# Performance work log

Measured on AMD Instinct MI355X. Metric: run time of the kernel, lower is better.

Reference implementation:

```python
import jax, jax.numpy as jnp
import numpy as np

L, N, C, OPL = 20, 512, 10, 13        # levels, nodes/level, conditions/node, condition op length
HID, MID = 512, 256                   # hidden_dim, hid_dim
OP_DIM, EX_DIM, SAMP_DIM = 15, 108, 1000
EPS = 1e-5


def _lstm_cell(x, h, c, wih, whh, bih, bhh):
    gates = x @ wih.T + h @ whh.T + bih + bhh
    i, f, g, o = jnp.split(gates, 4, axis=-1)  # torch gate order i,f,g,o
    c = jax.nn.sigmoid(f) * c + jax.nn.sigmoid(i) * jnp.tanh(g)
    h = jax.nn.sigmoid(o) * jnp.tanh(c)
    return h, c


def _batchnorm(x, g, b):  # training-mode BatchNorm1d (biased batch stats)
    m = x.mean(0)
    v = x.var(0)
    return (x - m) / jnp.sqrt(v + EPS) * g + b


def setup_inputs() -> dict:
    key = jax.random.key(0)
    ks = iter(jax.random.split(key, 48))
    rn = lambda shp, s=1.0: jax.random.normal(next(ks), shp, jnp.float32) * s
    ru = lambda shp: jax.random.uniform(next(ks), shp, jnp.float32)
    w = lambda shp: rn(shp, 0.05)
    inp = {
        'operators': ru((L, N, OP_DIM)),
        'extra_infos': rn((L, N, EX_DIM)),
        'condition1s': rn((L, N, C, OPL)),
        'condition2s': rn((L, N, C, OPL)),
        'samples': ru((L, N, SAMP_DIM)),
        'condition_masks': jnp.ones((L, N, 1), jnp.float32),
        'mapping': jax.random.randint(next(ks), (L, 2, N), 0, N + 1),
        # lstm1 (condition encoder)
        'w_ih1': w((4 * HID, OPL)), 'w_hh1': w((4 * HID, HID)),
        'b_ih1': w((4 * HID,)), 'b_hh1': w((4 * HID,)),
        # mlps feeding the tree lstm
        'sample_w': w((MID, SAMP_DIM)), 'sample_b': w((MID,)),
        'cond_w': w((MID, HID)), 'cond_b': w((MID,)),
        'bn1_g': jnp.ones((MID,), jnp.float32), 'bn1_b': jnp.zeros((MID,), jnp.float32),
        # lstm2 (tree aggregation)
        'w_ih2': w((4 * HID, OP_DIM + EX_DIM + 2 * MID)), 'w_hh2': w((4 * HID, HID)),
        'b_ih2': w((4 * HID,)), 'b_hh2': w((4 * HID,)),
        'bn2_g': jnp.ones((HID,), jnp.float32), 'bn2_b': jnp.zeros((HID,), jnp.float32),
        # task heads
        't1_w2': w((MID, HID)), 't1_b2': w((MID,)),
        't2_w2': w((MID, HID)), 't2_b2': w((MID,)),
        'bn3_g': jnp.ones((MID,), jnp.float32), 'bn3_b': jnp.zeros((MID,), jnp.float32),
        't1_w3': w((MID, MID)), 't1_b3': w((MID,)),
        't2_w3': w((MID, MID)), 't2_b3': w((MID,)),
        't1_ow': w((1, MID)), 't1_ob': w((1,)),
        't2_ow': w((1, MID)), 't2_ob': w((1,)),
    }
    return inp


def reference(operators, extra_infos, condition1s, condition2s, samples, condition_masks, mapping,
              w_ih1, w_hh1, b_ih1, b_hh1, sample_w, sample_b, cond_w, cond_b, bn1_g, bn1_b,
              w_ih2, w_hh2, b_ih2, b_hh2, bn2_g, bn2_b,
              t1_w2, t1_b2, t2_w2, t2_b2, bn3_g, bn3_b,
              t1_w3, t1_b3, t2_w3, t2_b3, t1_ow, t1_ob, t2_ow, t2_ob):
    Lv, Np = operators.shape[0], operators.shape[1]
    mapping = mapping.astype(jnp.int32)

    # --- condition encoder: lstm1 over each node's predicate sequence ---
    x = condition1s.reshape(Lv * Np, C, OPL)
    h0 = jnp.zeros((Lv * Np, HID), operators.dtype)

    def step1(carry, xt):
        h, c = carry
        h, c = _lstm_cell(xt, h, c, w_ih1, w_hh1, b_ih1, b_hh1)
        return (h, c), None

    (h_last, _), _ = jax.lax.scan(step1, (h0, h0), jnp.swapaxes(x, 0, 1))
    cond = _batchnorm(jax.nn.relu(h_last @ cond_w.T + cond_b), bn1_g, bn1_b)
    cond = cond.reshape(Lv, Np, MID)

    samp = jax.nn.relu(samples @ sample_w.T + sample_b) * condition_masks
    feats = jnp.concatenate([operators, extra_infos, cond, samp], axis=2)  # [L, N, 123+2*MID]

    # --- bottom level: lstm2 single step from zero state ---
    z0 = jnp.zeros((Np, HID), feats.dtype)
    hid, cid = _lstm_cell(feats[Lv - 1], z0, z0, w_ih2, w_hh2, b_ih2, b_hh2)

    # --- bottom-up tree aggregation: gather children states, average, lstm2 step ---
    def level_step(carry, inputs):
        hid, cid = carry
        x_lvl, mapp = inputs  # x_lvl [N, F], mapp [2, N], index 0 == pad (no child)
        pad = jnp.zeros((1, HID), hid.dtype)
        nh = jnp.concatenate([pad, hid], axis=0)  # [N+1, H]
        nc = jnp.concatenate([pad, cid], axis=0)
        h = (nh[mapp[0]] + nh[mapp[1]]) * 0.5
        c = (nc[mapp[0]] + nc[mapp[1]]) * 0.5
        hid, cid = _lstm_cell(x_lvl, h, c, w_ih2, w_hh2, b_ih2, b_hh2)
        return (hid, cid), None

    xs = (feats[Lv - 2::-1], mapping[Lv - 2::-1])
    (hid, cid), _ = jax.lax.scan(level_step, (hid, cid), xs)

    # --- heads (batch_size == Np: all level-0 nodes active for these inputs) ---
    z = _batchnorm(hid, bn2_g, bn2_b)
    t1 = _batchnorm(jax.nn.relu(z @ t1_w2.T + t1_b2), bn3_g, bn3_b)
    t1 = jax.nn.sigmoid(jax.nn.relu(t1 @ t1_w3.T + t1_b3) @ t1_ow.T + t1_ob)
    t2 = _batchnorm(jax.nn.relu(z @ t2_w2.T + t2_b2), bn3_g, bn3_b)
    t2 = jax.nn.sigmoid(jax.nn.relu(t2 @ t2_w3.T + t2_b3) @ t2_ow.T + t2_ob)
    return t1, t2
```

## Files before the change

kernel.cpp:

```cpp
#include <hip/hip_runtime.h>
#include <hip/hip_bf16.h>


typedef __bf16 bf16x8 __attribute__((ext_vector_type(8)));
typedef float f32x4 __attribute__((ext_vector_type(4)));

#define MROWS 10240
#define LDH1  552
#define L1_ROWS 48
#define L1_BLOCKS 214

#define PF_BIAS1   0
#define PF_BIAS2   2048
#define PF_CONDB   4096
#define PF_SAMPB   4352
#define PF_BCAT2   4608
#define PF_B3CAT   5120
#define PF_BN1G    5632
#define PF_BN1B    5888
#define PF_BN2G    6144
#define PF_BN2B    6656
#define PF_BN3G    7168
#define PF_BN3B    7424
#define PF_OW      7680
#define PF_OB      8192
#define PF_TOTAL   8194

__device__ __forceinline__ float fsig(float x) {
  return __builtin_amdgcn_rcpf(1.0f + __expf(-x));
}
__device__ __forceinline__ float ftanh(float x) {
  return fmaf(2.0f, __builtin_amdgcn_rcpf(1.0f + __expf(-2.0f * x)), -1.0f);
}
__device__ __forceinline__ bf16x8 bzero8() {
  bf16x8 z;
#pragma unroll
  for (int i = 0; i < 8; ++i) z[i] = (__bf16)0.0f;
  return z;
}
__device__ __forceinline__ float ld_in(const void* p, long i, int bf) {
  return bf ? (float)((const __bf16*)p)[i] : ((const float*)p)[i];
}

__global__ void detect_kernel(const unsigned* __restrict__ masks, int* __restrict__ flag) {
  if (blockIdx.x == 0 && threadIdx.x == 0)
    *flag = (masks[0] == 0x3F803F80u) ? 1 : 0;
}

__global__ void prep_kernel(const int* __restrict__ flagp,
    const void* w_ih1, const void* w_hh1, const void* b_ih1, const void* b_hh1,
    const void* w_ih2, const void* w_hh2, const void* b_ih2, const void* b_hh2,
    const void* t1_w2, const void* t2_w2, const void* t1_b2, const void* t2_b2,
    const void* cond_w, const void* cond_b, const void* sample_w, const void* sample_b,
    const void* bn1_g, const void* bn1_b, const void* bn2_g, const void* bn2_b,
    const void* bn3_g, const void* bn3_b,
    const void* t1_w3, const void* t1_b3, const void* t2_w3, const void* t2_b3,
    const void* t1_ow, const void* t1_ob, const void* t2_ow, const void* t2_ob,
    const void* masks,
    __bf16* __restrict__ w1s, __bf16* __restrict__ w2s,
    __bf16* __restrict__ wcat2, __bf16* __restrict__ cond_w_bf,
    __bf16* __restrict__ sample_w_bf, __bf16* __restrict__ w3cat_bf,
    float* __restrict__ mask_f, float* __restrict__ pf)
{
  const int bf = *flagp;
  const int S1 = 2048 * 544;
  const int S2 = 2048 * 1152;
  const int S3 = 512 * 512;
  const int S4 = 256 * 512;
  const int S5 = 256 * 1000;
  const int S6 = 512 * 256;
  const int S7 = 10240;
  const int total = S1 + S2 + S3 + S4 + S5 + S6 + S7 + PF_TOTAL;
  for (int idx = blockIdx.x * blockDim.x + threadIdx.x; idx < total;
       idx += gridDim.x * blockDim.x) {
    int i = idx;
    if (i < S1) {
      int e = i & 7, l = (i >> 3) & 63, g = (i >> 9) & 3;
      int grp = i >> 11;
      int kk = grp % 17, cgt = grp / 17;
      int colq = l & 15, quad = l >> 4;
      int row = g * 512 + cgt * 16 + colq;
      int k = kk * 32 + quad * 8 + e;
      float v = (k < 512) ? ld_in(w_hh1, (long)row * 512 + k, bf)
              : (k < 525) ? ld_in(w_ih1, (long)row * 13 + (k - 512), bf) : 0.0f;
      w1s[i] = (__bf16)v;
      continue;
    }
    i -= S1;
    if (i < S2) {
      int e = i & 7, l = (i >> 3) & 63, g = (i >> 9) & 3;
      int grp = i >> 11;
      int kk = grp % 36, jt = grp / 36;
      int colq = l & 15, quad = l >> 4;
      int row = g * 512 + jt * 16 + colq;
      int k = kk * 32 + quad * 8 + e;
      float v = (k < 635) ? ld_in(w_ih2, (long)row * 635 + k, bf)
              : (k < 640) ? 0.0f : ld_in(w_hh2, (long)row * 512 + (k - 640), bf);
      w2s[i] = (__bf16)v;
      continue;
    }
    i -= S2;
    if (i < S3) {
      int r = i >> 9, k = i & 511;
      wcat2[i] = (__bf16)((r < 256) ? ld_in(t1_w2, r * 512 + k, bf)
                                    : ld_in(t2_w2, (r - 256) * 512 + k, bf));
      continue;
    }
    i -= S3;
    if (i < S4) { cond_w_bf[i] = (__bf16)ld_in(cond_w, i, bf); continue; }
    i -= S4;
    if (i < S5) { sample_w_bf[i] = (__bf16)ld_in(sample_w, i, bf); continue; }
    i -= S5;
    if (i < S6) {
      int r = i >> 8, k = i & 255;
      w3cat_bf[i] = (__bf16)((r < 256) ? ld_in(t1_w3, r * 256 + k, bf)
                                       : ld_in(t2_w3, (r - 256) * 256 + k, bf));
      continue;
    }
    i -= S6;
    if (i < S7) { mask_f[i] = ld_in(masks, i, bf); continue; }
    i -= S7;
    {
      int j = i;
      float v;
      if      (j < 2048) v = ld_in(b_ih1, j, bf) + ld_in(b_hh1, j, bf);
      else if (j < 4096) v = ld_in(b_ih2, j - 2048, bf) + ld_in(b_hh2, j - 2048, bf);
      else if (j < 4352) v = ld_in(cond_b, j - 4096, bf);
      else if (j < 4608) v = ld_in(sample_b, j - 4352, bf);
      else if (j < 5120) { int k = j - 4608; v = (k < 256) ? ld_in(t1_b2, k, bf) : ld_in(t2_b2, k - 256, bf); }
      else if (j < 5632) { int k = j - 5120; v = (k < 256) ? ld_in(t1_b3, k, bf) : ld_in(t2_b3, k - 256, bf); }
      else if (j < 5888) v = ld_in(bn1_g, j - 5632, bf);
      else if (j < 6144) v = ld_in(bn1_b, j - 5888, bf);
      else if (j < 6656) v = ld_in(bn2_g, j - 6144, bf);
      else if (j < 7168) v = ld_in(bn2_b, j - 6656, bf);
      else if (j < 7424) v = ld_in(bn3_g, j - 7168, bf);
      else if (j < 7680) v = ld_in(bn3_b, j - 7424, bf);
      else if (j < 8192) { int k = j - 7680; v = (k < 256) ? ld_in(t1_ow, k, bf) : ld_in(t2_ow, k - 256, bf); }
      else v = (j == 8192) ? ld_in(t1_ob, 0, bf) : ld_in(t2_ob, 0, bf);
      pf[j] = v;
    }
  }
}

__global__ void conv_samples_kernel(const int* __restrict__ flagp,
                                    const void* __restrict__ samples,
                                    __bf16* __restrict__ dst)
{
  const int bf = *flagp;
  if (bf) return;
  for (long i = blockIdx.x * blockDim.x + threadIdx.x; i < 10240000L;
       i += (long)gridDim.x * blockDim.x)
    dst[i] = (__bf16)ld_in(samples, i, bf);
}

__global__ void featcopy_kernel(const int* __restrict__ flagp,
                                const void* __restrict__ ops,
                                const void* __restrict__ extra,
                                __bf16* __restrict__ Astage)
{
  const int bf = *flagp;
  int idx = blockIdx.x * blockDim.x + threadIdx.x;
  int m = idx >> 7, c = idx & 127;
  float v; int col;
  if (c < 15)       { v = ld_in(ops, (long)m * 15 + c, bf);            col = c; }
  else if (c < 123) { v = ld_in(extra, (long)m * 108 + (c - 15), bf);  col = c; }
  else              { v = 0.0f;                                        col = 512 + c; }
  Astage[(size_t)m * 640 + col] = (__bf16)v;
}

__global__ __launch_bounds__(1024, 4) void lstm1_kernel(
    const int* __restrict__ flagp,
    const void* __restrict__ cond1,
    const __bf16* __restrict__ w1s,
    const float*  __restrict__ bias,
    __bf16* __restrict__ h_out)
{
  __shared__ __attribute__((aligned(16))) __bf16 hbuf[2][L1_ROWS * LDH1];
  const int bf   = *flagp;
  const int tid  = threadIdx.x;
  const int wave = tid >> 6;
  const int lane = tid & 63;
  const int colq = lane & 15;
  const int quad = lane >> 4;
  const int r0   = blockIdx.x * L1_ROWS;

  {
    bf16x8 z8 = bzero8();
    for (int i = tid * 8; i < 2 * L1_ROWS * LDH1; i += 1024 * 8)
      *(bf16x8*)&hbuf[0][i] = z8;
  }
  __syncthreads();
  if (tid < L1_ROWS * 8) {
    int row = tid >> 3, jj = tid & 7;
    int gr = r0 + row;
    if (gr < MROWS) {
      long base = (long)gr * 130;
      hbuf[0][row * LDH1 + 512 + jj] = (__bf16)ld_in(cond1, base + jj, bf);
      if (jj < 5) hbuf[0][row * LDH1 + 520 + jj] = (__bf16)ld_in(cond1, base + 8 + jj, bf);
    }
  }
  __syncthreads();

  float c_reg[2][3][4];
#pragma unroll
  for (int a = 0; a < 2; ++a)
#pragma unroll
    for (int b = 0; b < 3; ++b)
#pragma unroll
      for (int r = 0; r < 4; ++r) c_reg[a][b][r] = 0.0f;

  const int jbase = wave * 32;

  float bI[2], bF[2], bG[2], bO[2];
#pragma unroll
  for (int cg = 0; cg < 2; ++cg) {
    const int j = jbase + cg * 16 + colq;
    bI[cg] = bias[j];
    bF[cg] = bias[512 + j];
    bG[cg] = bias[1024 + j];
    bO[cg] = bias[1536 + j];
  }

#pragma unroll 1
  for (int t = 0; t < 10; ++t) {
    const __bf16* hcur = hbuf[t & 1];
    __bf16* hnxt = hbuf[(t + 1) & 1];
#pragma unroll
    for (int cg = 0; cg < 2; ++cg) {
      const int jc = jbase + cg * 16;
      f32x4 acc[3][4];
#pragma unroll
      for (int a = 0; a < 3; ++a)
#pragma unroll
        for (int g = 0; g < 4; ++g)
#pragma unroll
          for (int r = 0; r < 4; ++r) acc[a][g][r] = 0.0f;

      const __bf16* wp = w1s + ((size_t)(wave * 2 + cg) * 17 * 4 * 512) + (lane << 3);
#pragma unroll 1
      for (int kk = 0; kk < 17; ++kk) {
        const int kof = (kk << 5) + (quad << 3);
        bf16x8 af[3];
#pragma unroll
        for (int rt = 0; rt < 3; ++rt)
          af[rt] = *(const bf16x8*)&hcur[(rt * 16 + colq) * LDH1 + kof];
        bf16x8 bfr[4];
#pragma unroll
        for (int g = 0; g < 4; ++g)
          bfr[g] = *(const bf16x8*)&wp[(kk * 4 + g) << 9];
#pragma unroll
        for (int g = 0; g < 4; ++g)
#pragma unroll
          for (int rt = 0; rt < 3; ++rt)
            acc[rt][g] = __builtin_amdgcn_mfma_f32_16x16x32_bf16(af[rt], bfr[g], acc[rt][g], 0, 0, 0);
      }
#pragma unroll
      for (int rt = 0; rt < 3; ++rt)
#pragma unroll
        for (int r = 0; r < 4; ++r) {
          float c = fsig(acc[rt][1][r] + bF[cg]) * c_reg[cg][rt][r]
                  + fsig(acc[rt][0][r] + bI[cg]) * ftanh(acc[rt][2][r] + bG[cg]);
          c_reg[cg][rt][r] = c;
          float h = fsig(acc[rt][3][r] + bO[cg]) * ftanh(c);
          hnxt[(rt * 16 + quad * 4 + r) * LDH1 + jc + colq] = (__bf16)h;
        }
    }
    if (t < 9 && tid < L1_ROWS * 8) {
      int row = tid >> 3, jj = tid & 7;
      int gr = r0 + row;
      if (gr < MROWS) {
        long base = ((long)gr * 10 + (t + 1)) * 13;
        hnxt[row * LDH1 + 512 + jj] = (__bf16)ld_in(cond1, base + jj, bf);
        if (jj < 5) hnxt[row * LDH1 + 520 + jj] = (__bf16)ld_in(cond1, base + 8 + jj, bf);
      }
    }
    __syncthreads();
  }

  for (int i = tid; i < L1_ROWS * 64; i += 1024) {
    int row = i >> 6;
    int cb  = (i & 63) << 3;
    *(bf16x8*)&h_out[(size_t)(r0 + row) * 512 + cb] = *(const bf16x8*)&hbuf[0][row * LDH1 + cb];
  }
}

template<int ACT, int OUTBF, int MASKED>
__global__ __launch_bounds__(256, 4) void gemm_kernel(
    const __bf16* __restrict__ A, int lda,
    const __bf16* __restrict__ W, int ldw,
    const float* __restrict__ bias,
    float* __restrict__ outf, __bf16* __restrict__ outb, int ldc,
    const float* __restrict__ mask, int K)
{
  const int tid  = threadIdx.x;
  const int wave = tid >> 6;
  const int lane = tid & 63;
  const int colq = lane & 15;
  const int quad = lane >> 4;
  const int m0 = blockIdx.y * 64 + (wave >> 1) * 32;
  const int n0 = blockIdx.x * 64 + (wave & 1) * 32;

  f32x4 acc[2][2];
#pragma unroll
  for (int a = 0; a < 2; ++a)
#pragma unroll
    for (int b = 0; b < 2; ++b)
#pragma unroll
      for (int r = 0; r < 4; ++r) acc[a][b][r] = 0.0f;

  const int nk = (K + 31) >> 5;
  for (int kk = 0; kk < nk; ++kk) {
    const int kof = (kk << 5) + (quad << 3);
    bf16x8 a0, a1, b0, b1;
    if (kof < K) {
      a0 = *(const bf16x8*)&A[(size_t)(m0 + colq) * lda + kof];
      a1 = *(const bf16x8*)&A[(size_t)(m0 + 16 + colq) * lda + kof];
      b0 = *(const bf16x8*)&W[(size_t)(n0 + colq) * ldw + kof];
      b1 = *(const bf16x8*)&W[(size_t)(n0 + 16 + colq) * ldw + kof];
    } else {
      a0 = bzero8(); a1 = a0; b0 = a0; b1 = a0;
    }
    acc[0][0] = __builtin_amdgcn_mfma_f32_16x16x32_bf16(a0, b0, acc[0][0], 0, 0, 0);
    acc[0][1] = __builtin_amdgcn_mfma_f32_16x16x32_bf16(a0, b1, acc[0][1], 0, 0, 0);
    acc[1][0] = __builtin_amdgcn_mfma_f32_16x16x32_bf16(a1, b0, acc[1][0], 0, 0, 0);
    acc[1][1] = __builtin_amdgcn_mfma_f32_16x16x32_bf16(a1, b1, acc[1][1], 0, 0, 0);
  }
#pragma unroll
  for (int ai = 0; ai < 2; ++ai)
#pragma unroll
    for (int bi = 0; bi < 2; ++bi) {
      const int col = n0 + bi * 16 + colq;
      const float bv = bias[col];
#pragma unroll
      for (int r = 0; r < 4; ++r) {
        const int row = m0 + ai * 16 + quad * 4 + r;
        float v = acc[ai][bi][r] + bv;
        if (ACT) v = fmaxf(v, 0.0f);
        if (MASKED) v *= mask[row];
        if (OUTBF) outb[(size_t)row * ldc + col] = (__bf16)v;
        else       outf[(size_t)row * ldc + col] = v;
      }
    }
}

__global__ __launch_bounds__(256, 4) void sampgemm_kernel(
    const int* __restrict__ flagp,
    const void* __restrict__ samples_raw,
    const __bf16* __restrict__ samp_bf,
    const __bf16* __restrict__ W,
    const float* __restrict__ bias,
    __bf16* __restrict__ outb,
    const float* __restrict__ mask)
{
  const __bf16* A = (*flagp) ? (const __bf16*)samples_raw : samp_bf;
  const int tid  = threadIdx.x;
  const int wave = tid >> 6;
  const int lane = tid & 63;
  const int colq = lane & 15;
  const int quad = lane >> 4;
  const int m0 = blockIdx.y * 64 + (wave >> 1) * 32;
  const int n0 = blockIdx.x * 64 + (wave & 1) * 32;
  const int K = 1000;

  f32x4 acc[2][2];
#pragma unroll
  for (int a = 0; a < 2; ++a)
#pragma unroll
    for (int b = 0; b < 2; ++b)
#pragma unroll
      for (int r = 0; r < 4; ++r) acc[a][b][r] = 0.0f;

  for (int kk = 0; kk < 32; ++kk) {
    const int kof = (kk << 5) + (quad << 3);
    bf16x8 a0, a1, b0, b1;
    if (kof < K) {
      a0 = *(const bf16x8*)&A[(size_t)(m0 + colq) * 1000 + kof];
      a1 = *(const bf16x8*)&A[(size_t)(m0 + 16 + colq) * 1000 + kof];
      b0 = *(const bf16x8*)&W[(size_t)(n0 + colq) * 1000 + kof];
      b1 = *(const bf16x8*)&W[(size_t)(n0 + 16 + colq) * 1000 + kof];
    } else {
      a0 = bzero8(); a1 = a0; b0 = a0; b1 = a0;
    }
    acc[0][0] = __builtin_amdgcn_mfma_f32_16x16x32_bf16(a0, b0, acc[0][0], 0, 0, 0);
    acc[0][1] = __builtin_amdgcn_mfma_f32_16x16x32_bf16(a0, b1, acc[0][1], 0, 0, 0);
    acc[1][0] = __builtin_amdgcn_mfma_f32_16x16x32_bf16(a1, b0, acc[1][0], 0, 0, 0);
    acc[1][1] = __builtin_amdgcn_mfma_f32_16x16x32_bf16(a1, b1, acc[1][1], 0, 0, 0);
  }
#pragma unroll
  for (int ai = 0; ai < 2; ++ai)
#pragma unroll
    for (int bi = 0; bi < 2; ++bi) {
      const int col = n0 + bi * 16 + colq;
      const float bv = bias[col];
#pragma unroll
      for (int r = 0; r < 4; ++r) {
        const int row = m0 + ai * 16 + quad * 4 + r;
        float v = fmaxf(acc[ai][bi][r] + bv, 0.0f) * mask[row];
        outb[(size_t)row * 640 + col] = (__bf16)v;
      }
    }
}

__global__ __launch_bounds__(256, 4) void treelvl_kernel(
    const __bf16* __restrict__ Alvl,
    const __bf16* __restrict__ w2s,
    const float* __restrict__ bias,
    const int* __restrict__ mapping,
    const __bf16* __restrict__ h_src, const float* __restrict__ c_src,
    __bf16* __restrict__ h_dst, float* __restrict__ c_dst,
    float* __restrict__ h_f32, int first)
{
  const int tid  = threadIdx.x;
  const int wv   = tid >> 6;
  const int lane = tid & 63;
  const int colq = lane & 15;
  const int quad = lane >> 4;
  const int jt = blockIdx.x;
  const int mt = blockIdx.y;
  const int rowA = mt * 64 + wv * 16 + colq;

  int i0 = 0, i1 = 0;
  if (!first) { i0 = mapping[rowA]; i1 = mapping[512 + rowA]; }
  const float s0 = (i0 > 0) ? 0.5f : 0.0f;
  const float s1 = (i1 > 0) ? 0.5f : 0.0f;
  const __bf16* h0p = h_src + (size_t)((i0 > 0 ? i0 : 1) - 1) * 512;
  const __bf16* h1p = h_src + (size_t)((i1 > 0 ? i1 : 1) - 1) * 512;

  f32x4 acc[4];
#pragma unroll
  for (int g = 0; g < 4; ++g)
#pragma unroll
    for (int r = 0; r < 4; ++r) acc[g][r] = 0.0f;

  const __bf16* wbase = w2s + (size_t)jt * 36 * 4 * 512 + (lane << 3);
  const __bf16* arow  = Alvl + (size_t)rowA * 640;

#pragma unroll 4
  for (int kk = 0; kk < 20; ++kk) {
    const int kof = (kk << 5) + (quad << 3);
    bf16x8 afr = *(const bf16x8*)&arow[kof];
    bf16x8 b0 = *(const bf16x8*)&wbase[(kk * 4 + 0) << 9];
    bf16x8 b1 = *(const bf16x8*)&wbase[(kk * 4 + 1) << 9];
    bf16x8 b2 = *(const bf16x8*)&wbase[(kk * 4 + 2) << 9];
    bf16x8 b3 = *(const bf16x8*)&wbase[(kk * 4 + 3) << 9];
    acc[0] = __builtin_amdgcn_mfma_f32_16x16x32_bf16(afr, b0, acc[0], 0, 0, 0);
    acc[1] = __builtin_amdgcn_mfma_f32_16x16x32_bf16(afr, b1, acc[1], 0, 0, 0);
    acc[2] = __builtin_amdgcn_mfma_f32_16x16x32_bf16(afr, b2, acc[2], 0, 0, 0);
    acc[3] = __builtin_amdgcn_mfma_f32_16x16x32_bf16(afr, b3, acc[3], 0, 0, 0);
  }
#pragma unroll 4
  for (int kk = 20; kk < 36; ++kk) {
    const int kh = ((kk - 20) << 5) + (quad << 3);
    bf16x8 v0 = *(const bf16x8*)&h0p[kh];
    bf16x8 v1 = *(const bf16x8*)&h1p[kh];
    bf16x8 afr;
#pragma unroll
    for (int e = 0; e < 8; ++e)
      afr[e] = (__bf16)((float)v0[e] * s0 + (float)v1[e] * s1);
    bf16x8 b0 = *(const bf16x8*)&wbase[(kk * 4 + 0) << 9];
    bf16x8 b1 = *(const bf16x8*)&wbase[(kk * 4 + 1) << 9];
    bf16x8 b2 = *(const bf16x8*)&wbase[(kk * 4 + 2) << 9];
    bf16x8 b3 = *(const bf16x8*)&wbase[(kk * 4 + 3) << 9];
    acc[0] = __builtin_amdgcn_mfma_f32_16x16x32_bf16(afr, b0, acc[0], 0, 0, 0);
    acc[1] = __builtin_amdgcn_mfma_f32_16x16x32_bf16(afr, b1, acc[1], 0, 0, 0);
    acc[2] = __builtin_amdgcn_mfma_f32_16x16x32_bf16(afr, b2, acc[2], 0, 0, 0);
    acc[3] = __builtin_amdgcn_mfma_f32_16x16x32_bf16(afr, b3, acc[3], 0, 0, 0);
  }

  const int j = jt * 16 + colq;
  const float bi  = bias[j];
  const float bff = bias[512 + j];
  const float bg  = bias[1024 + j];
  const float bo  = bias[1536 + j];
#pragma unroll
  for (int r = 0; r < 4; ++r) {
    const int mrow = mt * 64 + wv * 16 + quad * 4 + r;
    float ci = 0.0f;
    if (!first) {
      int a0 = mapping[mrow], a1 = mapping[512 + mrow];
      if (a0 > 0) ci += c_src[(size_t)(a0 - 1) * 512 + j];
      if (a1 > 0) ci += c_src[(size_t)(a1 - 1) * 512 + j];
      ci *= 0.5f;
    }
    float c = fsig(acc[1][r] + bff) * ci + fsig(acc[0][r] + bi) * ftanh(acc[2][r] + bg);
    float h = fsig(acc[3][r] + bo) * ftanh(c);
    h_dst[(size_t)mrow * 512 + j] = (__bf16)h;
    c_dst[(size_t)mrow * 512 + j] = c;
    h_f32[(size_t)mrow * 512 + j] = h;
  }
}

__global__ void stats1_kernel(const float* __restrict__ in, int ld, int N,
                              int rows_per_blk, float* __restrict__ partial)
{
  int b = blockIdx.x;
  int r0 = b * rows_per_blk;
  for (int c = threadIdx.x; c < N; c += blockDim.x) {
    float s = 0.0f, sq = 0.0f;
    for (int r = 0; r < rows_per_blk; ++r) {
      float v = in[(size_t)(r0 + r) * ld + c];
      s += v; sq += v * v;
    }
    partial[(size_t)(2 * b) * N + c] = s;
    partial[(size_t)(2 * b + 1) * N + c] = sq;
  }
}

__global__ void stats2_kernel(const float* __restrict__ partial, int nb, int N,
                              float invM, float* __restrict__ stats)
{
  int c = blockIdx.x * blockDim.x + threadIdx.x;
  if (c >= N) return;
  float s = 0.0f, sq = 0.0f;
  for (int b = 0; b < nb; ++b) {
    s  += partial[(size_t)(2 * b) * N + c];
    sq += partial[(size_t)(2 * b + 1) * N + c];
  }
  float mean = s * invM;
  float var  = sq * invM - mean * mean;
  stats[c]     = mean;
  stats[N + c] = rsqrtf(fmaxf(var, 0.0f) + 1e-5f);
}

__global__ void norm_kernel(const float* __restrict__ in, int ldin,
                            const float* __restrict__ stats, int N, int cshift, int gmask,
                            const float* __restrict__ g, const float* __restrict__ b,
                            __bf16* __restrict__ outp, int ldc, int total)
{
  for (int idx = blockIdx.x * blockDim.x + threadIdx.x; idx < total;
       idx += gridDim.x * blockDim.x) {
    int row = idx >> cshift;
    int c = idx & (N - 1);
    float v = (in[(size_t)row * ldin + c] - stats[c]) * stats[N + c];
    int gi = c & gmask;
    v = v * g[gi] + b[gi];
    outp[(size_t)row * ldc + c] = (__bf16)v;
  }
}

__global__ void head_kernel(const int* __restrict__ flagp,
                            const __bf16* __restrict__ tmp3,
                            const float* __restrict__ pf,
                            void* __restrict__ outp)
{
  const int bf = *flagp;
  int idx = blockIdx.x * blockDim.x + threadIdx.x;
  if (idx >= 1024) return;
  int which = idx >> 9;
  int n = idx & 511;
  const __bf16* row = tmp3 + (size_t)n * 512 + which * 256;
  const float* ow = pf + PF_OW + which * 256;
  float s = pf[PF_OB + which];
  for (int k = 0; k < 256; ++k) s += (float)row[k] * ow[k];
  float v = fsig(s);
  if (bf) ((__bf16*)outp)[idx] = (__bf16)v;
  else    ((float*)outp)[idx]  = v;
}

extern "C" void kernel_launch(void* const* d_in, const int* in_sizes, int n_in,
                              void* d_out, int out_size, void* d_ws, size_t ws_size,
                              hipStream_t stream) {
  const void* operators       = d_in[0];
  const void* extra_infos     = d_in[1];
  const void* condition1s     = d_in[2];
  const void* samples         = d_in[4];
  const void* condition_masks = d_in[5];
  const int*  mapping         = (const int*)d_in[6];
  (void)in_sizes; (void)n_in; (void)out_size; (void)ws_size;

  char* ws = (char*)d_ws;
  size_t off = 0;
  auto alloc = [&](size_t bytes) -> void* {
    void* p = ws + off;
    off += (bytes + 255) & ~(size_t)255;
    return p;
  };
  int*    flag     = (int*)   alloc(256);
  __bf16* w1s      = (__bf16*)alloc((size_t)2048 * 544 * 2);
  __bf16* w2s      = (__bf16*)alloc((size_t)2048 * 1152 * 2);
  __bf16* wcat2    = (__bf16*)alloc(512 * 512 * 2);
  __bf16* cond_w_bf   = (__bf16*)alloc(256 * 512 * 2);
  __bf16* sample_w_bf = (__bf16*)alloc(256 * 1000 * 2);
  __bf16* w3cat_bf    = (__bf16*)alloc(512 * 256 * 2);
  float*  mask_f   = (float*) alloc(10240 * 4);
  float*  pf       = (float*) alloc(PF_TOTAL * 4);
  __bf16* samp_bf  = (__bf16*)alloc((size_t)10240 * 1000 * 2);
  __bf16* h_last   = (__bf16*)alloc((size_t)10272 * 512 * 2);
  float*  condtmp  = (float*) alloc((size_t)10240 * 256 * 4);
  __bf16* Astage   = (__bf16*)alloc((size_t)20 * 512 * 640 * 2);
  __bf16* hs0      = (__bf16*)alloc(512 * 512 * 2);
  __bf16* hs1      = (__bf16*)alloc(512 * 512 * 2);
  float*  cs0      = (float*) alloc(512 * 512 * 4);
  float*  cs1      = (float*) alloc(512 * 512 * 4);
  float*  h_f32    = (float*) alloc(512 * 512 * 4);
  __bf16* zbuf     = (__bf16*)alloc(512 * 512 * 2);
  float*  tmp1     = (float*) alloc(512 * 512 * 4);
  __bf16* tmp2     = (__bf16*)alloc(512 * 512 * 2);
  __bf16* tmp3     = (__bf16*)alloc(512 * 512 * 2);
  float*  partial  = (float*) alloc(64 * 2 * 512 * 4);
  float*  statsb   = (float*) alloc(2 * 512 * 4);

  detect_kernel<<<1, 64, 0, stream>>>((const unsigned*)condition_masks, flag);
  prep_kernel<<<4096, 256, 0, stream>>>(flag,
      d_in[7], d_in[8], d_in[9], d_in[10],
      d_in[17], d_in[18], d_in[19], d_in[20],
      d_in[23], d_in[25], d_in[24], d_in[26],
      d_in[13], d_in[14], d_in[11], d_in[12],
      d_in[15], d_in[16], d_in[21], d_in[22],
      d_in[27], d_in[28],
      d_in[29], d_in[30], d_in[31], d_in[32],
      d_in[33], d_in[34], d_in[35], d_in[36],
      condition_masks,
      w1s, w2s, wcat2, cond_w_bf, sample_w_bf, w3cat_bf, mask_f, pf);
  conv_samples_kernel<<<4096, 256, 0, stream>>>(flag, samples, samp_bf);
  featcopy_kernel<<<5120, 256, 0, stream>>>(flag, operators, extra_infos, Astage);
  lstm1_kernel<<<L1_BLOCKS, 1024, 0, stream>>>(flag, condition1s, w1s, pf + PF_BIAS1, h_last);

  gemm_kernel<1,0,0><<<dim3(4,160), 256, 0, stream>>>(h_last, 512, cond_w_bf, 512,
      pf + PF_CONDB, condtmp, nullptr, 256, nullptr, 512);
  stats1_kernel<<<64, 256, 0, stream>>>(condtmp, 256, 256, 160, partial);
  stats2_kernel<<<1, 256, 0, stream>>>(partial, 64, 256, 1.0f / 10240.0f, statsb);
  norm_kernel<<<2560, 256, 0, stream>>>(condtmp, 256, statsb, 256, 8, 255,
      pf + PF_BN1G, pf + PF_BN1B, Astage + 123, 640, 10240 * 256);

  sampgemm_kernel<<<dim3(4,160), 256, 0, stream>>>(flag, samples, samp_bf,
      sample_w_bf, pf + PF_SAMPB, Astage + 379, mask_f);

  for (int lvl = 19; lvl >= 0; --lvl) {
    __bf16* hd = (lvl & 1) ? hs1 : hs0;
    float*  cd = (lvl & 1) ? cs1 : cs0;
    const __bf16* hsrc = (lvl & 1) ? hs0 : hs1;
    const float*  csrc = (lvl & 1) ? cs0 : cs1;
    treelvl_kernel<<<dim3(32,8), 256, 0, stream>>>(
        Astage + (size_t)lvl * 512 * 640, w2s, pf + PF_BIAS2,
        mapping + lvl * 1024, hsrc, csrc, hd, cd, h_f32, (lvl == 19) ? 1 : 0);
  }

  stats1_kernel<<<8, 256, 0, stream>>>(h_f32, 512, 512, 64, partial);
  stats2_kernel<<<2, 256, 0, stream>>>(partial, 8, 512, 1.0f / 512.0f, statsb);
  norm_kernel<<<256, 256, 0, stream>>>(h_f32, 512, statsb, 512, 9, 511,
      pf + PF_BN2G, pf + PF_BN2B, zbuf, 512, 512 * 512);

  gemm_kernel<1,0,0><<<dim3(8,8), 256, 0, stream>>>(zbuf, 512, wcat2, 512,
      pf + PF_BCAT2, tmp1, nullptr, 512, nullptr, 512);
  stats1_kernel<<<8, 256, 0, stream>>>(tmp1, 512, 512, 64, partial);
  stats2_kernel<<<2, 256, 0, stream>>>(partial, 8, 512, 1.0f / 512.0f, statsb);
  norm_kernel<<<256, 256, 0, stream>>>(tmp1, 512, statsb, 512, 9, 255,
      pf + PF_BN3G, pf + PF_BN3B, tmp2, 512, 512 * 512);

  gemm_kernel<1,1,0><<<dim3(4,8), 256, 0, stream>>>(tmp2, 512, w3cat_bf, 256,
      pf + PF_B3CAT, nullptr, tmp3, 512, nullptr, 256);
  gemm_kernel<1,1,0><<<dim3(4,8), 256, 0, stream>>>(tmp2 + 256, 512, w3cat_bf + 256 * 256, 256,
      pf + PF_B3CAT + 256, nullptr, tmp3 + 256, 512, nullptr, 256);

  head_kernel<<<4, 256, 0, stream>>>(flag, tmp3, pf, d_out);
}
```

Before: 1.027 ms.

## Fuse tree-level LSTM launches into one cooperative kernel with grid sync

Replaces 20 per-level tree LSTM kernel launches with a single cooperative kernel that loops over levels and uses grid.sync between them. Launch overhead and inter-kernel gaps are removed, and the f32 hidden copy is written only at the final level. The cost is a grid-wide barrier per level, and the kernel requires all 256 blocks to be co-resident. It also drops __restrict__ qualifiers, which may affect codegen.

```diff
diff --git a/kernel.cpp b/kernel.cpp
--- a/kernel.cpp
+++ b/kernel.cpp
@@ -1,5 +1,8 @@
 #include <hip/hip_runtime.h>
 #include <hip/hip_bf16.h>
+#include <hip/hip_cooperative_groups.h>
+
+namespace cg = cooperative_groups;
 
 
 typedef __bf16 bf16x8 __attribute__((ext_vector_type(8)));
@@ -401,15 +404,16 @@
     }
 }
 
-__global__ __launch_bounds__(256, 4) void treelvl_kernel(
-    const __bf16* __restrict__ Alvl,
-    const __bf16* __restrict__ w2s,
-    const float* __restrict__ bias,
-    const int* __restrict__ mapping,
-    const __bf16* __restrict__ h_src, const float* __restrict__ c_src,
-    __bf16* __restrict__ h_dst, float* __restrict__ c_dst,
-    float* __restrict__ h_f32, int first)
-{
+__global__ __launch_bounds__(256, 4) void tree_kernel(
+    const __bf16* Astage,
+    const __bf16* w2s,
+    const float*  bias,
+    const int*    mapping_all,
+    __bf16* hs0, __bf16* hs1,
+    float*  cs0, float*  cs1,
+    float*  h_f32)
+{
+  cg::grid_group grid = cg::this_grid();
   const int tid  = threadIdx.x;
   const int wv   = tid >> 6;
   const int lane = tid & 63;
@@ -418,75 +422,90 @@
   const int jt = blockIdx.x;
   const int mt = blockIdx.y;
   const int rowA = mt * 64 + wv * 16 + colq;
-
-  int i0 = 0, i1 = 0;
-  if (!first) { i0 = mapping[rowA]; i1 = mapping[512 + rowA]; }
-  const float s0 = (i0 > 0) ? 0.5f : 0.0f;
-  const float s1 = (i1 > 0) ? 0.5f : 0.0f;
-  const __bf16* h0p = h_src + (size_t)((i0 > 0 ? i0 : 1) - 1) * 512;
-  const __bf16* h1p = h_src + (size_t)((i1 > 0 ? i1 : 1) - 1) * 512;
-
-  f32x4 acc[4];
-#pragma unroll
-  for (int g = 0; g < 4; ++g)
-#pragma unroll
-    for (int r = 0; r < 4; ++r) acc[g][r] = 0.0f;
+  const int mrow0 = mt * 64 + wv * 16 + quad * 4;
 
   const __bf16* wbase = w2s + (size_t)jt * 36 * 4 * 512 + (lane << 3);
-  const __bf16* arow  = Alvl + (size_t)rowA * 640;
-
-#pragma unroll 4
-  for (int kk = 0; kk < 20; ++kk) {
-    const int kof = (kk << 5) + (quad << 3);
-    bf16x8 afr = *(const bf16x8*)&arow[kof];
-    bf16x8 b0 = *(const bf16x8*)&wbase[(kk * 4 + 0) << 9];
-    bf16x8 b1 = *(const bf16x8*)&wbase[(kk * 4 + 1) << 9];
-    bf16x8 b2 = *(const bf16x8*)&wbase[(kk * 4 + 2) << 9];
-    bf16x8 b3 = *(const bf16x8*)&wbase[(kk * 4 + 3) << 9];
-    acc[0] = __builtin_amdgcn_mfma_f32_16x16x32_bf16(afr, b0, acc[0], 0, 0, 0);
-    acc[1] = __builtin_amdgcn_mfma_f32_16x16x32_bf16(afr, b1, acc[1], 0, 0, 0);
-    acc[2] = __builtin_amdgcn_mfma_f32_16x16x32_bf16(afr, b2, acc[2], 0, 0, 0);
-    acc[3] = __builtin_amdgcn_mfma_f32_16x16x32_bf16(afr, b3, acc[3], 0, 0, 0);
-  }
-#pragma unroll 4
-  for (int kk = 20; kk < 36; ++kk) {
-    const int kh = ((kk - 20) << 5) + (quad << 3);
-    bf16x8 v0 = *(const bf16x8*)&h0p[kh];
-    bf16x8 v1 = *(const bf16x8*)&h1p[kh];
-    bf16x8 afr;
-#pragma unroll
-    for (int e = 0; e < 8; ++e)
-      afr[e] = (__bf16)((float)v0[e] * s0 + (float)v1[e] * s1);
-    bf16x8 b0 = *(const bf16x8*)&wbase[(kk * 4 + 0) << 9];
-    bf16x8 b1 = *(const bf16x8*)&wbase[(kk * 4 + 1) << 9];
-    bf16x8 b2 = *(const bf16x8*)&wbase[(kk * 4 + 2) << 9];
-    bf16x8 b3 = *(const bf16x8*)&wbase[(kk * 4 + 3) << 9];
-    acc[0] = __builtin_amdgcn_mfma_f32_16x16x32_bf16(afr, b0, acc[0], 0, 0, 0);
-    acc[1] = __builtin_amdgcn_mfma_f32_16x16x32_bf16(afr, b1, acc[1], 0, 0, 0);
-    acc[2] = __builtin_amdgcn_mfma_f32_16x16x32_bf16(afr, b2, acc[2], 0, 0, 0);
-    acc[3] = __builtin_amdgcn_mfma_f32_16x16x32_bf16(afr, b3, acc[3], 0, 0, 0);
-  }
-
   const int j = jt * 16 + colq;
   const float bi  = bias[j];
   const float bff = bias[512 + j];
   const float bg  = bias[1024 + j];
   const float bo  = bias[1536 + j];
-#pragma unroll
-  for (int r = 0; r < 4; ++r) {
-    const int mrow = mt * 64 + wv * 16 + quad * 4 + r;
-    float ci = 0.0f;
-    if (!first) {
-      int a0 = mapping[mrow], a1 = mapping[512 + mrow];
-      if (a0 > 0) ci += c_src[(size_t)(a0 - 1) * 512 + j];
-      if (a1 > 0) ci += c_src[(size_t)(a1 - 1) * 512 + j];
-      ci *= 0.5f;
-    }
-    float c = fsig(acc[1][r] + bff) * ci + fsig(acc[0][r] + bi) * ftanh(acc[2][r] + bg);
-    float h = fsig(acc[3][r] + bo) * ftanh(c);
-    h_dst[(size_t)mrow * 512 + j] = (__bf16)h;
-    c_dst[(size_t)mrow * 512 + j] = c;
-    h_f32[(size_t)mrow * 512 + j] = h;
+
+#pragma unroll 1
+  for (int lvl = 19; lvl >= 0; --lvl) {
+    const int first = (lvl == 19);
+    const __bf16* Alvl = Astage + (size_t)lvl * 512 * 640;
+    const int* mapping = mapping_all + lvl * 1024;
+    __bf16* h_dst = (lvl & 1) ? hs1 : hs0;
+    float*  c_dst = (lvl & 1) ? cs1 : cs0;
+    const __bf16* h_src = (lvl & 1) ? hs0 : hs1;
+    const float*  c_src = (lvl & 1) ? cs0 : cs1;
+
+    int i0 = 0, i1 = 0;
+    if (!first) { i0 = mapping[rowA]; i1 = mapping[512 + rowA]; }
+    const float s0 = (i0 > 0) ? 0.5f : 0.0f;
+    const float s1 = (i1 > 0) ? 0.5f : 0.0f;
+    const __bf16* h0p = h_src + (size_t)((i0 > 0 ? i0 : 1) - 1) * 512;
+    const __bf16* h1p = h_src + (size_t)((i1 > 0 ? i1 : 1) - 1) * 512;
+
+    f32x4 acc[4];
+#pragma unroll
+    for (int g = 0; g < 4; ++g)
+#pragma unroll
+      for (int r = 0; r < 4; ++r) acc[g][r] = 0.0f;
+
+    const __bf16* arow = Alvl + (size_t)rowA * 640;
+
+#pragma unroll 4
+    for (int kk = 0; kk < 20; ++kk) {
+      const int kof = (kk << 5) + (quad << 3);
+      bf16x8 afr = *(const bf16x8*)&arow[kof];
+      bf16x8 b0 = *(const bf16x8*)&wbase[(kk * 4 + 0) << 9];
+      bf16x8 b1 = *(const bf16x8*)&wbase[(kk * 4 + 1) << 9];
+      bf16x8 b2 = *(const bf16x8*)&wbase[(kk * 4 + 2) << 9];
+      bf16x8 b3 = *(const bf16x8*)&wbase[(kk * 4 + 3) << 9];
+      acc[0] = __builtin_amdgcn_mfma_f32_16x16x32_bf16(afr, b0, acc[0], 0, 0, 0);
+      acc[1] = __builtin_amdgcn_mfma_f32_16x16x32_bf16(afr, b1, acc[1], 0, 0, 0);
+      acc[2] = __builtin_amdgcn_mfma_f32_16x16x32_bf16(afr, b2, acc[2], 0, 0, 0);
+      acc[3] = __builtin_amdgcn_mfma_f32_16x16x32_bf16(afr, b3, acc[3], 0, 0, 0);
+    }
+#pragma unroll 4
+    for (int kk = 20; kk < 36; ++kk) {
+      const int kh = ((kk - 20) << 5) + (quad << 3);
+      bf16x8 v0 = *(const bf16x8*)&h0p[kh];
+      bf16x8 v1 = *(const bf16x8*)&h1p[kh];
+      bf16x8 afr;
+#pragma unroll
+      for (int e = 0; e < 8; ++e)
+        afr[e] = (__bf16)((float)v0[e] * s0 + (float)v1[e] * s1);
+      bf16x8 b0 = *(const bf16x8*)&wbase[(kk * 4 + 0) << 9];
+      bf16x8 b1 = *(const bf16x8*)&wbase[(kk * 4 + 1) << 9];
+      bf16x8 b2 = *(const bf16x8*)&wbase[(kk * 4 + 2) << 9];
+      bf16x8 b3 = *(const bf16x8*)&wbase[(kk * 4 + 3) << 9];
+      acc[0] = __builtin_amdgcn_mfma_f32_16x16x32_bf16(afr, b0, acc[0], 0, 0, 0);
+      acc[1] = __builtin_amdgcn_mfma_f32_16x16x32_bf16(afr, b1, acc[1], 0, 0, 0);
+      acc[2] = __builtin_amdgcn_mfma_f32_16x16x32_bf16(afr, b2, acc[2], 0, 0, 0);
+      acc[3] = __builtin_amdgcn_mfma_f32_16x16x32_bf16(afr, b3, acc[3], 0, 0, 0);
+    }
+
+#pragma unroll
+    for (int r = 0; r < 4; ++r) {
+      const int mrow = mrow0 + r;
+      float ci = 0.0f;
+      if (!first) {
+        int a0 = mapping[mrow], a1 = mapping[512 + mrow];
+        if (a0 > 0) ci += c_src[(size_t)(a0 - 1) * 512 + j];
+        if (a1 > 0) ci += c_src[(size_t)(a1 - 1) * 512 + j];
+        ci *= 0.5f;
+      }
+      float c = fsig(acc[1][r] + bff) * ci + fsig(acc[0][r] + bi) * ftanh(acc[2][r] + bg);
+      float h = fsig(acc[3][r] + bo) * ftanh(c);
+      h_dst[(size_t)mrow * 512 + j] = (__bf16)h;
+      c_dst[(size_t)mrow * 512 + j] = c;
+      if (lvl == 0) h_f32[(size_t)mrow * 512 + j] = h;
+    }
+
+    if (lvl > 0) grid.sync();
   }
 }
 
@@ -626,14 +645,19 @@
   sampgemm_kernel<<<dim3(4,160), 256, 0, stream>>>(flag, samples, samp_bf,
       sample_w_bf, pf + PF_SAMPB, Astage + 379, mask_f);
 
-  for (int lvl = 19; lvl >= 0; --lvl) {
-    __bf16* hd = (lvl & 1) ? hs1 : hs0;
-    float*  cd = (lvl & 1) ? cs1 : cs0;
-    const __bf16* hsrc = (lvl & 1) ? hs0 : hs1;
-    const float*  csrc = (lvl & 1) ? cs0 : cs1;
-    treelvl_kernel<<<dim3(32,8), 256, 0, stream>>>(
-        Astage + (size_t)lvl * 512 * 640, w2s, pf + PF_BIAS2,
-        mapping + lvl * 1024, hsrc, csrc, hd, cd, h_f32, (lvl == 19) ? 1 : 0);
+  {
+    const __bf16* tAst = Astage;
+    const __bf16* tW   = w2s;
+    const float*  tB   = pf + PF_BIAS2;
+    const int*    tMap = mapping;
+    __bf16* th0 = hs0; __bf16* th1 = hs1;
+    float*  tc0 = cs0; float*  tc1 = cs1;
+    float*  thf = h_f32;
+    void* targs[] = { (void*)&tAst, (void*)&tW, (void*)&tB, (void*)&tMap,
+                      (void*)&th0, (void*)&th1, (void*)&tc0, (void*)&tc1,
+                      (void*)&thf };
+    hipLaunchCooperativeKernel((const void*)tree_kernel,
+                               dim3(32, 8), dim3(256, 1, 1), targs, 0, stream);
   }
 
   stats1_kernel<<<8, 256, 0, stream>>>(h_f32, 512, 512, 64, partial);
```

Result: slower. 1.732 ms (+68.6%).
